# Kernel optimization log

Hardware: AMD Instinct MI355X
Metric: run time of the kernel (lower is better)

Reference implementation:

```python
import jax, jax.numpy as jnp
import numpy as np
from jax import lax

B, S, T = 32, 100, 4
NUM_C2, NUM_C3, NUM_D, DV = 500, 2000, 1000, 128


def setup_inputs():
    key = jax.random.key(0)
    ks = jax.random.split(key, 25)
    s = 0.05
    def nrm(k, shape):
        return jax.random.normal(k, shape, dtype=jnp.float32) * s
    return {
        "c2_seq": jax.random.randint(ks[0], (B, S), 0, NUM_C2),
        "c3_seq": jax.random.randint(ks[1], (B, S, T), 1, NUM_C3 + 1),  # 0 is padding; use all-valid tags
        "d_seq": jax.random.randint(ks[2], (B, S), 0, NUM_D),
        "r_seq": jax.random.randint(ks[3], (B, S), 0, 2),
        "D_emb": nrm(ks[4], (NUM_D, 1)),
        "R_emb": nrm(ks[5], (2, DV)),
        "v_c2": nrm(ks[6], (DV,)),
        "v_c3": nrm(ks[7], (DV,)),
        "v_d": nrm(ks[8], (DV,)),
        "W_ih": nrm(ks[9], (3 * DV, 2 * DV)),
        "W_hh": nrm(ks[10], (3 * DV, DV)),
        "b_ih": nrm(ks[11], (3 * DV,)),
        "b_hh": nrm(ks[12], (3 * DV,)),
        "l1_W1": nrm(ks[13], (DV, DV)), "l1_b1": nrm(ks[14], (DV,)),
        "l1_W2": nrm(ks[15], (1, DV)), "l1_b2": nrm(ks[16], (1,)),
        "l2_W1": nrm(ks[17], (DV, 4 * DV)), "l2_b1": nrm(ks[18], (DV,)),
        "l2_W2": nrm(ks[19], (1, DV)), "l2_b2": nrm(ks[20], (1,)),
        "l3_W1": nrm(ks[21], (DV, 4 * DV)), "l3_b1": nrm(ks[22], (DV,)),
        "l3_W2": nrm(ks[23], (1, DV)), "l3_b2": nrm(ks[24], (1,)),
    }


def _mlp(x, W1, b1, W2, b2):
    # Linear -> ReLU -> (Dropout: identity in eval) -> Linear -> (Dropout)
    return jnp.maximum(x @ W1.T + b1, 0.0) @ W2.T + b2


def _gru(x_seq, h0, W_ih, W_hh, b_ih, b_hh):
    # torch.nn.GRU math, batch_first
    def step(h, x):
        gi = x @ W_ih.T + b_ih
        gh = h @ W_hh.T + b_hh
        i_r, i_z, i_n = jnp.split(gi, 3, axis=-1)
        h_r, h_z, h_n = jnp.split(gh, 3, axis=-1)
        r = jax.nn.sigmoid(i_r + h_r)
        z = jax.nn.sigmoid(i_z + h_z)
        n = jnp.tanh(i_n + r * h_n)
        h_new = (1.0 - z) * n + z * h
        return h_new, h_new
    _, hs = lax.scan(step, h0, jnp.swapaxes(x_seq, 0, 1))
    return jnp.swapaxes(hs, 0, 1)


def _forward(c2_seq, c3_seq, d_seq, r_seq, p):
    (D_emb, R_emb, v_c2, v_c3, v_d, W_ih, W_hh, b_ih, b_hh,
     l1_W1, l1_b1, l1_W2, l1_b2, l2_W1, l2_b1, l2_W2, l2_b2,
     l3_W1, l3_b1, l3_W2, l3_b2) = p
    Bn = c2_seq.shape[0]
    gamma = D_emb[d_seq]                      # [B,S,1]
    v_d_seq = gamma * v_d                     # [B,S,DV]
    v_r_seq = R_emb[r_seq]                    # [B,S,DV]
    h0 = jnp.zeros((Bn, DV), dtype=v_d_seq.dtype)
    h_seq = _gru(jnp.concatenate([v_d_seq, v_r_seq], -1), h0, W_ih, W_hh, b_ih, b_hh)
    alpha_seq = _mlp(h_seq, l1_W1, l1_b1, l1_W2, l1_b2)[..., 0]   # [B,S]

    def step(carry, xs):
        C2, C3 = carry
        c2, c3, vd, vr = xs                                      # [B],[B,T],[B,DV],[B,DV]
        mask = (c3 != 0).astype(C3.dtype)                        # [B,T]
        w = mask / mask.sum(-1, keepdims=True)
        beta2 = jnp.take_along_axis(C2, c2[:, None], axis=-1)    # [B,1]
        beta3 = jnp.take_along_axis(C3, c3, axis=-1)             # [B,T]
        beta3_bar = (beta3 * w).sum(-1)                          # [B]
        vc2 = beta2 * v_c2                                       # [B,DV]
        vc3 = beta3[..., None] * v_c3                            # [B,T,DV]
        vc3_bar = beta3_bar[:, None] * v_c3                      # [B,DV]
        new_c2 = _mlp(jnp.concatenate([vc2, vc3_bar, vd, vr], -1),
                      l2_W1, l2_b1, l2_W2, l2_b2)[:, 0]          # [B]
        feat3 = jnp.concatenate([
            jnp.broadcast_to(vc2[:, None, :], vc3.shape), vc3,
            jnp.broadcast_to(vd[:, None, :], vc3.shape),
            jnp.broadcast_to(vr[:, None, :], vc3.shape)], -1)    # [B,T,4*DV]
        new_c3 = _mlp(feat3, l3_W1, l3_b1, l3_W2, l3_b2)[..., 0]  # [B,T]
        oh2 = jax.nn.one_hot(c2, NUM_C2, dtype=C2.dtype)          # [B,NC2]
        oh3 = jax.nn.one_hot(c3, NUM_C3 + 1, dtype=C3.dtype) * mask[..., None]  # [B,T,NC3+1]
        multi = oh3.sum(1)
        C2n = C2 * (1.0 - oh2) + new_c2[:, None] * oh2
        C3n = C3 * (1.0 - multi) + (new_c3[..., None] * oh3).sum(1)
        return (C2n, C3n), (C2n, C3n)

    C2_0 = jnp.zeros((Bn, NUM_C2), dtype=jnp.float32)
    C3_0 = jnp.zeros((Bn, NUM_C3 + 1), dtype=jnp.float32)
    xs = (jnp.swapaxes(c2_seq, 0, 1), jnp.swapaxes(c3_seq, 0, 1),
          jnp.swapaxes(v_d_seq, 0, 1), jnp.swapaxes(v_r_seq, 0, 1))
    _, (C2_seq, C3_seq) = lax.scan(step, (C2_0, C3_0), xs)
    C2_seq = jnp.swapaxes(C2_seq, 0, 1)   # [B,S,NUM_C2]
    C3_seq = jnp.swapaxes(C3_seq, 0, 1)   # [B,S,NUM_C3+1]
    return alpha_seq, h_seq, C2_seq, C3_seq


def reference(c2_seq, c3_seq, d_seq, r_seq, D_emb, R_emb, v_c2, v_c3, v_d,
              W_ih, W_hh, b_ih, b_hh, l1_W1, l1_b1, l1_W2, l1_b2,
              l2_W1, l2_b1, l2_W2, l2_b2, l3_W1, l3_b1, l3_W2, l3_b2):
    p = (D_emb, R_emb, v_c2, v_c3, v_d, W_ih, W_hh, b_ih, b_hh,
         l1_W1, l1_b1, l1_W2, l1_b2, l2_W1, l2_b1, l2_W2, l2_b2,
         l3_W1, l3_b1, l3_W2, l3_b2)
    return _forward(c2_seq, c3_seq, d_seq, r_seq, p)
```

## Files before the change

kernel.cpp:

```cpp
#include <hip/hip_runtime.h>

#define BB   32
#define SS   100
#define TT   4
#define NCC2 500
#define NC3P 2001
#define DD   128

#define LDSF 14664

typedef _Float16 h2v __attribute__((ext_vector_type(2)));

__device__ __forceinline__ float fast_rcp(float x) { return __builtin_amdgcn_rcpf(x); }
__device__ __forceinline__ float fast_sig(float x) { return fast_rcp(1.f + __expf(-x)); }
__device__ __forceinline__ float fast_tanh(float x) { return 1.f - 2.f * fast_rcp(__expf(2.f * x) + 1.f); }

__device__ __forceinline__ float dpp_sum64(float x) {
    x += __int_as_float(__builtin_amdgcn_update_dpp(0, __float_as_int(x), 0x111, 0xf, 0xf, true));
    x += __int_as_float(__builtin_amdgcn_update_dpp(0, __float_as_int(x), 0x112, 0xf, 0xf, true));
    x += __int_as_float(__builtin_amdgcn_update_dpp(0, __float_as_int(x), 0x114, 0xf, 0xf, true));
    x += __int_as_float(__builtin_amdgcn_update_dpp(0, __float_as_int(x), 0x118, 0xf, 0xf, true));
    x += __int_as_float(__builtin_amdgcn_update_dpp(0, __float_as_int(x), 0x142, 0xa, 0xf, true));
    x += __int_as_float(__builtin_amdgcn_update_dpp(0, __float_as_int(x), 0x143, 0xc, 0xf, true));
    return x;
}

__device__ __forceinline__ float dpp_sum16(float x) {
    x += __int_as_float(__builtin_amdgcn_update_dpp(0, __float_as_int(x), 0x111, 0xf, 0xf, true));
    x += __int_as_float(__builtin_amdgcn_update_dpp(0, __float_as_int(x), 0x112, 0xf, 0xf, true));
    x += __int_as_float(__builtin_amdgcn_update_dpp(0, __float_as_int(x), 0x114, 0xf, 0xf, true));
    x += __int_as_float(__builtin_amdgcn_update_dpp(0, __float_as_int(x), 0x118, 0xf, 0xf, true));
    return x;
}

__device__ __forceinline__ float dot4(float4 a, float4 b) {
    return fmaf(a.x, b.x, fmaf(a.y, b.y, fmaf(a.z, b.z, a.w * b.w)));
}

__device__ __forceinline__ unsigned pk16(float a, float b) {
    return __builtin_bit_cast(unsigned, __builtin_amdgcn_cvt_pkrtz(a, b));
}
__device__ __forceinline__ uint4 packf16(float4 A, float4 B) {
    uint4 u;
    u.x = pk16(A.x, A.y); u.y = pk16(A.z, A.w);
    u.z = pk16(B.x, B.y); u.w = pk16(B.z, B.w);
    return u;
}

#define MIX8(q, u, v, acc) do {                                             \
    h2v _x;                                                                 \
    _x = __builtin_bit_cast(h2v, (q).x);                                    \
    acc = fmaf((float)_x.x, (u).x, acc); acc = fmaf((float)_x.y, (u).y, acc);\
    _x = __builtin_bit_cast(h2v, (q).y);                                    \
    acc = fmaf((float)_x.x, (u).z, acc); acc = fmaf((float)_x.y, (u).w, acc);\
    _x = __builtin_bit_cast(h2v, (q).z);                                    \
    acc = fmaf((float)_x.x, (v).x, acc); acc = fmaf((float)_x.y, (v).y, acc);\
    _x = __builtin_bit_cast(h2v, (q).w);                                    \
    acc = fmaf((float)_x.x, (v).z, acc); acc = fmaf((float)_x.y, (v).w, acc);\
} while (0)

__global__ __launch_bounds__(768, 1) void k_main(
    const int* __restrict__ c2_seq, const int* __restrict__ c3_seq,
    const int* __restrict__ d_seq,  const int* __restrict__ r_seq,
    const float* __restrict__ D_emb, const float* __restrict__ Remb,
    const float* __restrict__ v_c2, const float* __restrict__ v_c3,
    const float* __restrict__ v_d,
    const float* __restrict__ W_ih, const float* __restrict__ W_hh,
    const float* __restrict__ b_ih, const float* __restrict__ b_hh,
    const float* __restrict__ l2W1, const float* __restrict__ l2b1,
    const float* __restrict__ l2W2, const float* __restrict__ l2b2,
    const float* __restrict__ l3W1, const float* __restrict__ l3b1,
    const float* __restrict__ l3W2, const float* __restrict__ l3b2,
    float* __restrict__ h_out, float* __restrict__ C2o, float* __restrict__ C3o)
{
    __shared__ __align__(16) float sh[LDSF];
    int* shi = (int*)sh;
    float4* sh4 = (float4*)sh;
    const int blk = blockIdx.x;
    const int t = threadIdx.x;

    if (blk < BB) {
        const int b  = blk;
        const int w  = t >> 6, l = t & 63;
        const int p4 = w & 3;
        const int j2 = (w >> 2) * 64 + l;
        const int jA = j2, jB = j2 + 192;
        const int kb = p4 * 32;

        uint4 wa0, wa1, wa2, wa3, wb0, wb1, wb2, wb3;
        {
            const float4* ra = (const float4*)(W_hh + jA * DD + kb);
            const float4* rb = (const float4*)(W_hh + jB * DD + kb);
            wa0 = packf16(ra[0], ra[1]); wa1 = packf16(ra[2], ra[3]);
            wa2 = packf16(ra[4], ra[5]); wa3 = packf16(ra[6], ra[7]);
            wb0 = packf16(rb[0], rb[1]); wb1 = packf16(rb[2], rb[3]);
            wb2 = packf16(rb[4], rb[5]); wb3 = packf16(rb[6], rb[7]);
        }

        {
            const float4* vd4 = (const float4*)(v_d + kb);
            const float4* r04 = (const float4*)(Remb + kb);
            const float4* r14 = (const float4*)(Remb + 128 + kb);
#pragma unroll
            for (int rr2 = 0; rr2 < 2; ++rr2) {
                const int j = rr2 ? jB : jA;
                const float4* wx = (const float4*)(W_ih + j * 256 + kb);
                const float4* wr = (const float4*)(W_ih + j * 256 + 128 + kb);
                float pd = 0.f, pr0 = 0.f, pr1 = 0.f;
#pragma unroll
                for (int i = 0; i < 8; ++i) {
                    float4 a = wx[i], c = wr[i];
                    float4 vd = vd4[i], r0 = r04[i], r1 = r14[i];
                    pd  = fmaf(a.x, vd.x, fmaf(a.y, vd.y, fmaf(a.z, vd.z, fmaf(a.w, vd.w, pd))));
                    pr0 = fmaf(c.x, r0.x, fmaf(c.y, r0.y, fmaf(c.z, r0.z, fmaf(c.w, r0.w, pr0))));
                    pr1 = fmaf(c.x, r1.x, fmaf(c.y, r1.y, fmaf(c.z, r1.z, fmaf(c.w, r1.w, pr1))));
                }
                sh[1864 + j * 4 + p4] = pd;
                sh[3400 + j * 4 + p4] = pr0;
                sh[4936 + j * 4 + p4] = pr1;
            }
        }
        if (t < SS) {
            sh[1664 + t]  = D_emb[d_seq[b * SS + t]];
            shi[1764 + t] = r_seq[b * SS + t];
        }
        __syncthreads();

        float gd_r=0,gd_z=0,gd_n=0, g0_r=0,g0_z=0,g0_n=0, g1_r=0,g1_z=0,g1_n=0;
        float bi_r=0,bi_z=0,bi_n=0, bh_r=0,bh_z=0,bh_n=0, h = 0.f;
        if (t < DD) {
            float4 a;
            a = sh4[466 + t];        gd_r = (a.x+a.y)+(a.z+a.w);
            a = sh4[466 + 128 + t];  gd_z = (a.x+a.y)+(a.z+a.w);
            a = sh4[466 + 256 + t];  gd_n = (a.x+a.y)+(a.z+a.w);
            a = sh4[850 + t];        g0_r = (a.x+a.y)+(a.z+a.w);
            a = sh4[850 + 128 + t];  g0_z = (a.x+a.y)+(a.z+a.w);
            a = sh4[850 + 256 + t];  g0_n = (a.x+a.y)+(a.z+a.w);
            a = sh4[1234 + t];       g1_r = (a.x+a.y)+(a.z+a.w);
            a = sh4[1234 + 128 + t]; g1_z = (a.x+a.y)+(a.z+a.w);
            a = sh4[1234 + 256 + t]; g1_n = (a.x+a.y)+(a.z+a.w);
            bi_r = b_ih[t]; bi_z = b_ih[t+128]; bi_n = b_ih[t+256];
            bh_r = b_hh[t]; bh_z = b_hh[t+128]; bh_n = b_hh[t+256];
            sh[t] = 0.f;
        }
        __syncthreads();

        for (int s = 0; s < SS; ++s) {
            float aA = 0.f, aB = 0.f;
            {
                const float4* hq = sh4 + p4 * 8;
                float4 h0 = hq[0], h1 = hq[1], h2 = hq[2], h3 = hq[3];
                float4 h4 = hq[4], h5 = hq[5], h6 = hq[6], h7 = hq[7];
                MIX8(wa0, h0, h1, aA); MIX8(wa1, h2, h3, aA);
                MIX8(wa2, h4, h5, aA); MIX8(wa3, h6, h7, aA);
                MIX8(wb0, h0, h1, aB); MIX8(wb1, h2, h3, aB);
                MIX8(wb2, h4, h5, aB); MIX8(wb3, h6, h7, aB);
            }
            sh[128 + jA * 4 + p4] = aA;
            sh[128 + jB * 4 + p4] = aB;
            __syncthreads();
            if (t < DD) {
                float4 q0 = sh4[32 + t];
                float4 q1 = sh4[32 + 128 + t];
                float4 q2 = sh4[32 + 256 + t];
                float ghr = (q0.x+q0.y)+(q0.z+q0.w) + bh_r;
                float ghz = (q1.x+q1.y)+(q1.z+q1.w) + bh_z;
                float ghn = (q2.x+q2.y)+(q2.z+q2.w) + bh_n;
                float gamma = sh[1664 + s]; int rr = shi[1764 + s];
                float gir = fmaf(gamma, gd_r, (rr ? g1_r : g0_r) + bi_r);
                float giz = fmaf(gamma, gd_z, (rr ? g1_z : g0_z) + bi_z);
                float gin = fmaf(gamma, gd_n, (rr ? g1_n : g0_n) + bi_n);
                float r = fast_sig(gir + ghr);
                float z = fast_sig(giz + ghz);
                float n = fast_tanh(fmaf(r, ghn, gin));
                h = (1.f - z) * n + z * h;
                sh[t] = h;
                sh[1864 + s * DD + t] = h;
            }
            __syncthreads();
        }

        {
            const float4* hs = (const float4*)(sh + 1864);
            float4* hd = (float4*)(h_out + (size_t)b * SS * DD);
            for (int i = t; i < SS * DD / 4; i += 768) hd[i] = hs[i];
        }
    } else {
        const int sb = blk - BB;
        const int b = sb >> 2;
        const int q = sb & 3;

        {
            const int g = (t & 63) >> 4, c8 = ((t & 63) & 15) * 8;
            const float* vsrc = (g == 0) ? v_c2 : (g == 1) ? v_c3 : (g == 2) ? v_d : Remb;
            const float4 va  = *(const float4*)(vsrc + c8);
            const float4 vb  = *(const float4*)(vsrc + c8 + 4);
            const float4 va1 = *(const float4*)(Remb + 128 + c8);
            const float4 vb1 = *(const float4*)(Remb + 132 + c8);
            for (int r = t >> 6; r < 256; r += 12) {
                const float* W = (r < 128) ? l2W1 : l3W1;
                float* U = sh + ((r < 128) ? 3264 : 3904);
                const int i = r & 127;
                const float* wr = W + i * 512 + g * 128 + c8;
                const float4 w0 = *(const float4*)(wr);
                const float4 w1 = *(const float4*)(wr + 4);
                float p  = dot4(w0, va)  + dot4(w1, vb);
                float p1 = dot4(w0, va1) + dot4(w1, vb1);
                p  = dpp_sum16(p);
                p1 = dpp_sum16(p1);
                if ((t & 15) == 15) {
                    U[g * 128 + i] = p;
                    if (g == 3) U[512 + i] = p1;
                }
            }
        }
        for (int k = t; k < NCC2 + NC3P; k += 768) sh[k] = 0.f;
        for (int k = t; k < SS; k += 768) {
            shi[2504 + k] = c2_seq[b * SS + k];
            sh[3004 + k]  = D_emb[d_seq[b * SS + k]];
            shi[3104 + k] = r_seq[b * SS + k];
        }
        for (int k = t; k < SS; k += 768)
            reinterpret_cast<int4*>(shi + 2604)[k] = reinterpret_cast<const int4*>(c3_seq + b * SS * TT)[k];
        __syncthreads();
        if (t >= 64) return;

        float* C2s = sh;
        float* C3s = sh + NCC2;
        const float* u2 = sh + 3264;
        const float* u3 = sh + 3904;
        const float u2a0 = u2[t],        u2a1 = u2[64 + t];
        const float u2b0 = u2[128 + t],  u2b1 = u2[192 + t];
        const float u2c0 = u2[256 + t],  u2c1 = u2[320 + t];
        const float u2d00 = u2[384 + t], u2d01 = u2[448 + t];
        const float u2d10 = u2[512 + t], u2d11 = u2[576 + t];
        const float u3a0 = u3[t],        u3a1 = u3[64 + t];
        const float u3b0 = u3[128 + t],  u3b1 = u3[192 + t];
        const float u3c0 = u3[256 + t],  u3c1 = u3[320 + t];
        const float u3d00 = u3[384 + t], u3d01 = u3[448 + t];
        const float u3d10 = u3[512 + t], u3d11 = u3[576 + t];
        const float b2_0 = l2b1[t], b2_1 = l2b1[64 + t];
        const float w2_0 = l2W2[t], w2_1 = l2W2[64 + t];
        const float b3_0 = l3b1[t], b3_1 = l3b1[64 + t];
        const float w3_0 = l3W2[t], w3_1 = l3W2[64 + t];
        const float c2bias = l2b2[0], c3bias = l3b2[0];

        int  nc2 = shi[2504];
        int4 nc3 = reinterpret_cast<const int4*>(shi + 2604)[0];
        float ngam = sh[3004];
        int   nrr  = shi[3104];

        for (int s = 0; s < SS; ++s) {
            const int rs = b * SS + s;
            const int c2i = nc2;
            const int i0 = nc3.x, i1 = nc3.y, i2 = nc3.z, i3 = nc3.w;
            const float gamma = ngam;
            const int rr = nrr;
            if (s + 1 < SS) {
                nc2 = shi[2504 + s + 1];
                nc3 = reinterpret_cast<const int4*>(shi + 2604)[s + 1];
                ngam = sh[3004 + s + 1];
                nrr  = shi[3104 + s + 1];
            }

            const float beta2 = C2s[c2i];
            const bool k0 = (i0 != 0), k1 = (i1 != 0), k2 = (i2 != 0), k3 = (i3 != 0);
            const float m0 = k0 ? 1.f : 0.f, m1 = k1 ? 1.f : 0.f;
            const float m2 = k2 ? 1.f : 0.f, m3 = k3 ? 1.f : 0.f;
            const float bt0 = C3s[i0], bt1 = C3s[i1], bt2 = C3s[i2], bt3 = C3s[i3];
            const float msum = m0 + m1 + m2 + m3;
            const float b3bar = (bt0 * m0 + bt1 * m1 + bt2 * m2 + bt3 * m3) * fast_rcp(msum);

            const float ud20 = rr ? u2d10 : u2d00, ud21 = rr ? u2d11 : u2d01;
            const float ud30 = rr ? u3d10 : u3d00, ud31 = rr ? u3d11 : u3d01;

            float h20 = fmaf(beta2, u2a0, fmaf(b3bar, u2b0, fmaf(gamma, u2c0, ud20 + b2_0)));
            float h21 = fmaf(beta2, u2a1, fmaf(b3bar, u2b1, fmaf(gamma, u2c1, ud21 + b2_1)));
            float newc2 = dpp_sum64(fmaf(fmaxf(h20, 0.f), w2_0, fmaxf(h21, 0.f) * w2_1)) + c2bias;

            const float base30 = fmaf(beta2, u3a0, fmaf(gamma, u3c0, ud30 + b3_0));
            const float base31 = fmaf(beta2, u3a1, fmaf(gamma, u3c1, ud31 + b3_1));
            float ha, hb, q0, q1, q2, q3;
            ha = fmaf(bt0, u3b0, base30); hb = fmaf(bt0, u3b1, base31);
            q0 = dpp_sum64(fmaf(fmaxf(ha, 0.f), w3_0, fmaxf(hb, 0.f) * w3_1)) + c3bias;
            ha = fmaf(bt1, u3b0, base30); hb = fmaf(bt1, u3b1, base31);
            q1 = dpp_sum64(fmaf(fmaxf(ha, 0.f), w3_0, fmaxf(hb, 0.f) * w3_1)) + c3bias;
            ha = fmaf(bt2, u3b0, base30); hb = fmaf(bt2, u3b1, base31);
            q2 = dpp_sum64(fmaf(fmaxf(ha, 0.f), w3_0, fmaxf(hb, 0.f) * w3_1)) + c3bias;
            ha = fmaf(bt3, u3b0, base30); hb = fmaf(bt3, u3b1, base31);
            q3 = dpp_sum64(fmaf(fmaxf(ha, 0.f), w3_0, fmaxf(hb, 0.f) * w3_1)) + c3bias;

            float val0, val1, val2, val3;
            {
                float c = m0 + ((k1 && i1 == i0) ? 1.f : 0.f) + ((k2 && i2 == i0) ? 1.f : 0.f) + ((k3 && i3 == i0) ? 1.f : 0.f);
                float qs = (k0 ? q0 : 0.f) + ((k1 && i1 == i0) ? q1 : 0.f) + ((k2 && i2 == i0) ? q2 : 0.f) + ((k3 && i3 == i0) ? q3 : 0.f);
                val0 = bt0 * (1.f - c) + qs;
            }
            {
                float c = ((k0 && i0 == i1) ? 1.f : 0.f) + m1 + ((k2 && i2 == i1) ? 1.f : 0.f) + ((k3 && i3 == i1) ? 1.f : 0.f);
                float qs = ((k0 && i0 == i1) ? q0 : 0.f) + (k1 ? q1 : 0.f) + ((k2 && i2 == i1) ? q2 : 0.f) + ((k3 && i3 == i1) ? q3 : 0.f);
                val1 = bt1 * (1.f - c) + qs;
            }
            {
                float c = ((k0 && i0 == i2) ? 1.f : 0.f) + ((k1 && i1 == i2) ? 1.f : 0.f) + m2 + ((k3 && i3 == i2) ? 1.f : 0.f);
                float qs = ((k0 && i0 == i2) ? q0 : 0.f) + ((k1 && i1 == i2) ? q1 : 0.f) + (k2 ? q2 : 0.f) + ((k3 && i3 == i2) ? q3 : 0.f);
                val2 = bt2 * (1.f - c) + qs;
            }
            {
                float c = ((k0 && i0 == i3) ? 1.f : 0.f) + ((k1 && i1 == i3) ? 1.f : 0.f) + ((k2 && i2 == i3) ? 1.f : 0.f) + m3;
                float qs = ((k0 && i0 == i3) ? q0 : 0.f) + ((k1 && i1 == i3) ? q1 : 0.f) + ((k2 && i2 == i3) ? q2 : 0.f) + (k3 ? q3 : 0.f);
                val3 = bt3 * (1.f - c) + qs;
            }

            if (t == 63) {
                C2s[c2i] = newc2;
                if (k0) C3s[i0] = val0;
                if (k1) C3s[i1] = val1;
                if (k2) C3s[i2] = val2;
                if (k3) C3s[i3] = val3;
            }

            if (q == 0) {
                float* c2row = C2o + (size_t)rs * NCC2;
                const float4* src = reinterpret_cast<const float4*>(C2s);
                float4* dst = reinterpret_cast<float4*>(c2row);
                dst[t] = src[t];
                if (t < 61) dst[64 + t] = src[64 + t];
            } else {
                float* c3row = C3o + (size_t)rs * NC3P;
                const int lo = (q - 1) * 667;
                const int n = 667;
                int pre = (4 - (int)(((unsigned)(rs * NC3P + lo)) & 3)) & 3;
                if (pre > n) pre = n;
                if (t < pre) c3row[lo + t] = C3s[lo + t];
                const int st = lo + pre;
                const int rem = n - pre;
                const int nv = rem >> 2, tl = rem & 3;
                for (int i = t; i < nv; i += 64) {
                    const int d = st + 4 * i;
                    *reinterpret_cast<float4*>(c3row + d) =
                        make_float4(C3s[d], C3s[d + 1], C3s[d + 2], C3s[d + 3]);
                }
                if (t < tl) {
                    const int d = st + 4 * nv + t;
                    c3row[d] = C3s[d];
                }
            }
        }
    }
}

__global__ __launch_bounds__(256) void k_alpha(const float* __restrict__ h_seq,
                                               const float* __restrict__ W1,
                                               const float* __restrict__ b1,
                                               const float* __restrict__ W2,
                                               const float* __restrict__ b2,
                                               float* __restrict__ alpha)
{
    __shared__ __align__(16) float sl[22560];
    const int t = threadIdx.x;
    const int base = blockIdx.x * 16;

    float4* hl4 = reinterpret_cast<float4*>(sl);
    const float4* hg = reinterpret_cast<const float4*>(h_seq + (size_t)base * DD);
    for (int i = t; i < 512; i += 256) hl4[i] = hg[i];

    float4* wl4 = reinterpret_cast<float4*>(sl + 6144);
    const float4* wg = reinterpret_cast<const float4*>(W1);
    for (int g = t; g < 4096; g += 256) {
        const int ch = g >> 5, k4 = g & 31;
        wl4[ch * 32 + (k4 ^ (ch & 31))] = wg[g];
    }
    __syncthreads();

    const int ch = t & 127, half = t >> 7;
    float acc[16];
#pragma unroll
    for (int r = 0; r < 16; ++r) acc[r] = 0.f;
#pragma unroll
    for (int kk = 0; kk < 16; ++kk) {
        const int k4 = half * 16 + kk;
        const float4 w = wl4[ch * 32 + (k4 ^ (ch & 31))];
#pragma unroll
        for (int r = 0; r < 16; ++r) {
            const float4 hv = hl4[r * 32 + k4];
            acc[r] = fmaf(w.x, hv.x, fmaf(w.y, hv.y, fmaf(w.z, hv.z, fmaf(w.w, hv.w, acc[r]))));
        }
    }
#pragma unroll
    for (int r = 0; r < 16; ++r) sl[2048 + r * 256 + t] = acc[r];
    __syncthreads();
    if (t < 128) {
        const float b1v = b1[t], w2v = W2[t];
#pragma unroll
        for (int r = 0; r < 16; ++r) {
            float v = fmaxf(sl[2048 + r * 256 + t] + sl[2048 + r * 256 + 128 + t] + b1v, 0.f) * w2v;
            v = dpp_sum64(v);
            if ((t & 63) == 63) sl[22528 + r * 2 + (t >> 6)] = v;
        }
    }
    __syncthreads();
    if (t < 16) alpha[base + t] = sl[22528 + 2 * t] + sl[22528 + 2 * t + 1] + b2[0];
}

extern "C" void kernel_launch(void* const* d_in, const int* in_sizes, int n_in,
                              void* d_out, int out_size, void* d_ws, size_t ws_size,
                              hipStream_t stream)
{
    (void)in_sizes; (void)n_in; (void)out_size; (void)d_ws; (void)ws_size;
    const int*   c2_seq = (const int*)d_in[0];
    const int*   c3_seq = (const int*)d_in[1];
    const int*   d_seq  = (const int*)d_in[2];
    const int*   r_seq  = (const int*)d_in[3];
    const float* D_emb  = (const float*)d_in[4];
    const float* Remb   = (const float*)d_in[5];
    const float* v_c2   = (const float*)d_in[6];
    const float* v_c3   = (const float*)d_in[7];
    const float* v_d    = (const float*)d_in[8];
    const float* W_ih   = (const float*)d_in[9];
    const float* W_hh   = (const float*)d_in[10];
    const float* b_ih   = (const float*)d_in[11];
    const float* b_hh   = (const float*)d_in[12];
    const float* l1W1   = (const float*)d_in[13];
    const float* l1b1   = (const float*)d_in[14];
    const float* l1W2   = (const float*)d_in[15];
    const float* l1b2   = (const float*)d_in[16];
    const float* l2W1   = (const float*)d_in[17];
    const float* l2b1   = (const float*)d_in[18];
    const float* l2W2   = (const float*)d_in[19];
    const float* l2b2   = (const float*)d_in[20];
    const float* l3W1   = (const float*)d_in[21];
    const float* l3b1   = (const float*)d_in[22];
    const float* l3W2   = (const float*)d_in[23];
    const float* l3b2   = (const float*)d_in[24];

    float* out   = (float*)d_out;
    float* alpha = out;
    float* h_out = out + 3200;
    float* C2o   = out + 412800;
    float* C3o   = out + 2012800;

    k_main<<<BB + 4 * BB, 768, 0, stream>>>(c2_seq, c3_seq, d_seq, r_seq, D_emb, Remb,
                                            v_c2, v_c3, v_d,
                                            W_ih, W_hh, b_ih, b_hh,
                                            l2W1, l2b1, l2W2, l2b2,
                                            l3W1, l3b1, l3W2, l3b2,
                                            h_out, C2o, C3o);
    k_alpha<<<200, 256, 0, stream>>>(h_out, l1W1, l1b1, l1W2, l1b2, alpha);
}
```

Measured before the change: 112.7 us.

## Decouple C2/C3 recurrence from row writeout and use all threads for stores

The scan blocks now run the sequential C2/C3 update on one wave and log per-step new values to LDS. Afterwards they replay those updates, and each of the four quarter-blocks writes full rows for every fourth step using all 768 threads, instead of one wave writing a column slice every step. The GRU blocks also change their partial-sum layout from interleaved float4 to a strided layout indexed by p4, and the sigmoid/tanh helpers are inlined. This is meant to take the large global writeout out of the serial dependency chain. In exchange it recomputes the same recurrence redundantly in four blocks and adds barriers inside the replay loop.

Result: slower. 118.3 us (+5.0%).

```diff
diff --git a/kernel.cpp b/kernel.cpp
--- a/kernel.cpp
+++ b/kernel.cpp
@@ -7,13 +7,11 @@
 #define NC3P 2001
 #define DD   128
 
-#define LDSF 14664
+#define LDSF 14680
 
 typedef _Float16 h2v __attribute__((ext_vector_type(2)));
 
 __device__ __forceinline__ float fast_rcp(float x) { return __builtin_amdgcn_rcpf(x); }
-__device__ __forceinline__ float fast_sig(float x) { return fast_rcp(1.f + __expf(-x)); }
-__device__ __forceinline__ float fast_tanh(float x) { return 1.f - 2.f * fast_rcp(__expf(2.f * x) + 1.f); }
 
 __device__ __forceinline__ float dpp_sum64(float x) {
     x += __int_as_float(__builtin_amdgcn_update_dpp(0, __float_as_int(x), 0x111, 0xf, 0xf, true));
@@ -115,30 +113,32 @@
                     pr0 = fmaf(c.x, r0.x, fmaf(c.y, r0.y, fmaf(c.z, r0.z, fmaf(c.w, r0.w, pr0))));
                     pr1 = fmaf(c.x, r1.x, fmaf(c.y, r1.y, fmaf(c.z, r1.z, fmaf(c.w, r1.w, pr1))));
                 }
-                sh[1864 + j * 4 + p4] = pd;
-                sh[3400 + j * 4 + p4] = pr0;
-                sh[4936 + j * 4 + p4] = pr1;
+                sh[1880 + p4 * 388 + j] = pd;
+                sh[3432 + p4 * 388 + j] = pr0;
+                sh[4984 + p4 * 388 + j] = pr1;
             }
         }
         if (t < SS) {
-            sh[1664 + t]  = D_emb[d_seq[b * SS + t]];
-            shi[1764 + t] = r_seq[b * SS + t];
+            sh[1680 + t]  = D_emb[d_seq[b * SS + t]];
+            shi[1780 + t] = r_seq[b * SS + t];
         }
         __syncthreads();
 
         float gd_r=0,gd_z=0,gd_n=0, g0_r=0,g0_z=0,g0_n=0, g1_r=0,g1_z=0,g1_n=0;
         float bi_r=0,bi_z=0,bi_n=0, bh_r=0,bh_z=0,bh_n=0, h = 0.f;
         if (t < DD) {
-            float4 a;
-            a = sh4[466 + t];        gd_r = (a.x+a.y)+(a.z+a.w);
-            a = sh4[466 + 128 + t];  gd_z = (a.x+a.y)+(a.z+a.w);
-            a = sh4[466 + 256 + t];  gd_n = (a.x+a.y)+(a.z+a.w);
-            a = sh4[850 + t];        g0_r = (a.x+a.y)+(a.z+a.w);
-            a = sh4[850 + 128 + t];  g0_z = (a.x+a.y)+(a.z+a.w);
-            a = sh4[850 + 256 + t];  g0_n = (a.x+a.y)+(a.z+a.w);
-            a = sh4[1234 + t];       g1_r = (a.x+a.y)+(a.z+a.w);
-            a = sh4[1234 + 128 + t]; g1_z = (a.x+a.y)+(a.z+a.w);
-            a = sh4[1234 + 256 + t]; g1_n = (a.x+a.y)+(a.z+a.w);
+#pragma unroll
+            for (int p = 0; p < 4; ++p) {
+                gd_r += sh[1880 + p * 388 + t];
+                gd_z += sh[1880 + p * 388 + 128 + t];
+                gd_n += sh[1880 + p * 388 + 256 + t];
+                g0_r += sh[3432 + p * 388 + t];
+                g0_z += sh[3432 + p * 388 + 128 + t];
+                g0_n += sh[3432 + p * 388 + 256 + t];
+                g1_r += sh[4984 + p * 388 + t];
+                g1_z += sh[4984 + p * 388 + 128 + t];
+                g1_n += sh[4984 + p * 388 + 256 + t];
+            }
             bi_r = b_ih[t]; bi_z = b_ih[t+128]; bi_n = b_ih[t+256];
             bh_r = b_hh[t]; bh_z = b_hh[t+128]; bh_n = b_hh[t+256];
             sh[t] = 0.f;
@@ -156,32 +156,33 @@
                 MIX8(wb0, h0, h1, aB); MIX8(wb1, h2, h3, aB);
                 MIX8(wb2, h4, h5, aB); MIX8(wb3, h6, h7, aB);
             }
-            sh[128 + jA * 4 + p4] = aA;
-            sh[128 + jB * 4 + p4] = aB;
+            sh[128 + p4 * 388 + jA] = aA;
+            sh[128 + p4 * 388 + jB] = aB;
             __syncthreads();
             if (t < DD) {
-                float4 q0 = sh4[32 + t];
-                float4 q1 = sh4[32 + 128 + t];
-                float4 q2 = sh4[32 + 256 + t];
-                float ghr = (q0.x+q0.y)+(q0.z+q0.w) + bh_r;
-                float ghz = (q1.x+q1.y)+(q1.z+q1.w) + bh_z;
-                float ghn = (q2.x+q2.y)+(q2.z+q2.w) + bh_n;
-                float gamma = sh[1664 + s]; int rr = shi[1764 + s];
+                float ghr = bh_r, ghz = bh_z, ghn = bh_n;
+#pragma unroll
+                for (int p = 0; p < 4; ++p) {
+                    ghr += sh[128 + p * 388 + t];
+                    ghz += sh[128 + p * 388 + 128 + t];
+                    ghn += sh[128 + p * 388 + 256 + t];
+                }
+                float gamma = sh[1680 + s]; int rr = shi[1780 + s];
                 float gir = fmaf(gamma, gd_r, (rr ? g1_r : g0_r) + bi_r);
                 float giz = fmaf(gamma, gd_z, (rr ? g1_z : g0_z) + bi_z);
                 float gin = fmaf(gamma, gd_n, (rr ? g1_n : g0_n) + bi_n);
-                float r = fast_sig(gir + ghr);
-                float z = fast_sig(giz + ghz);
-                float n = fast_tanh(fmaf(r, ghn, gin));
+                float r = fast_rcp(1.f + __expf(-(gir + ghr)));
+                float z = fast_rcp(1.f + __expf(-(giz + ghz)));
+                float n = 1.f - 2.f * fast_rcp(__expf(2.f * fmaf(r, ghn, gin)) + 1.f);
                 h = (1.f - z) * n + z * h;
                 sh[t] = h;
-                sh[1864 + s * DD + t] = h;
+                sh[1880 + s * DD + t] = h;
             }
             __syncthreads();
         }
 
         {
-            const float4* hs = (const float4*)(sh + 1864);
+            const float4* hs = (const float4*)(sh + 1880);
             float4* hd = (float4*)(h_out + (size_t)b * SS * DD);
             for (int i = t; i < SS * DD / 4; i += 768) hd[i] = hs[i];
         }
@@ -223,128 +224,144 @@
         for (int k = t; k < SS; k += 768)
             reinterpret_cast<int4*>(shi + 2604)[k] = reinterpret_cast<const int4*>(c3_seq + b * SS * TT)[k];
         __syncthreads();
-        if (t >= 64) return;
+
+        if (t < 64) {
+            float* C2s = sh;
+            float* C3s = sh + NCC2;
+            const float* u2 = sh + 3264;
+            const float* u3 = sh + 3904;
+            const float u2a0 = u2[t],        u2a1 = u2[64 + t];
+            const float u2b0 = u2[128 + t],  u2b1 = u2[192 + t];
+            const float u2c0 = u2[256 + t],  u2c1 = u2[320 + t];
+            const float u2d00 = u2[384 + t], u2d01 = u2[448 + t];
+            const float u2d10 = u2[512 + t], u2d11 = u2[576 + t];
+            const float u3a0 = u3[t],        u3a1 = u3[64 + t];
+            const float u3b0 = u3[128 + t],  u3b1 = u3[192 + t];
+            const float u3c0 = u3[256 + t],  u3c1 = u3[320 + t];
+            const float u3d00 = u3[384 + t], u3d01 = u3[448 + t];
+            const float u3d10 = u3[512 + t], u3d11 = u3[576 + t];
+            const float b2_0 = l2b1[t], b2_1 = l2b1[64 + t];
+            const float w2_0 = l2W2[t], w2_1 = l2W2[64 + t];
+            const float b3_0 = l3b1[t], b3_1 = l3b1[64 + t];
+            const float w3_0 = l3W2[t], w3_1 = l3W2[64 + t];
+            const float c2bias = l2b2[0], c3bias = l3b2[0];
+
+            int  nc2 = shi[2504];
+            int4 nc3 = reinterpret_cast<const int4*>(shi + 2604)[0];
+            float ngam = sh[3004];
+            int   nrr  = shi[3104];
+
+            for (int s = 0; s < SS; ++s) {
+                const int c2i = nc2;
+                const int i0 = nc3.x, i1 = nc3.y, i2 = nc3.z, i3 = nc3.w;
+                const float gamma = ngam;
+                const int rr = nrr;
+                if (s + 1 < SS) {
+                    nc2 = shi[2504 + s + 1];
+                    nc3 = reinterpret_cast<const int4*>(shi + 2604)[s + 1];
+                    ngam = sh[3004 + s + 1];
+                    nrr  = shi[3104 + s + 1];
+                }
+
+                const float beta2 = C2s[c2i];
+                const bool k0 = (i0 != 0), k1 = (i1 != 0), k2 = (i2 != 0), k3 = (i3 != 0);
+                const float m0 = k0 ? 1.f : 0.f, m1 = k1 ? 1.f : 0.f;
+                const float m2 = k2 ? 1.f : 0.f, m3 = k3 ? 1.f : 0.f;
+                const float bt0 = C3s[i0], bt1 = C3s[i1], bt2 = C3s[i2], bt3 = C3s[i3];
+                const float msum = m0 + m1 + m2 + m3;
+                const float b3bar = (bt0 * m0 + bt1 * m1 + bt2 * m2 + bt3 * m3) * fast_rcp(msum);
+
+                const float ud20 = rr ? u2d10 : u2d00, ud21 = rr ? u2d11 : u2d01;
+                const float ud30 = rr ? u3d10 : u3d00, ud31 = rr ? u3d11 : u3d01;
+
+                float h20 = fmaf(beta2, u2a0, fmaf(b3bar, u2b0, fmaf(gamma, u2c0, ud20 + b2_0)));
+                float h21 = fmaf(beta2, u2a1, fmaf(b3bar, u2b1, fmaf(gamma, u2c1, ud21 + b2_1)));
+                float newc2 = dpp_sum64(fmaf(fmaxf(h20, 0.f), w2_0, fmaxf(h21, 0.f) * w2_1)) + c2bias;
+
+                const float base30 = fmaf(beta2, u3a0, fmaf(gamma, u3c0, ud30 + b3_0));
+                const float base31 = fmaf(beta2, u3a1, fmaf(gamma, u3c1, ud31 + b3_1));
+                float ha, hb, q0, q1, q2, q3;
+                ha = fmaf(bt0, u3b0, base30); hb = fmaf(bt0, u3b1, base31);
+                q0 = dpp_sum64(fmaf(fmaxf(ha, 0.f), w3_0, fmaxf(hb, 0.f) * w3_1)) + c3bias;
+                ha = fmaf(bt1, u3b0, base30); hb = fmaf(bt1, u3b1, base31);
+                q1 = dpp_sum64(fmaf(fmaxf(ha, 0.f), w3_0, fmaxf(hb, 0.f) * w3_1)) + c3bias;
+                ha = fmaf(bt2, u3b0, base30); hb = fmaf(bt2, u3b1, base31);
+                q2 = dpp_sum64(fmaf(fmaxf(ha, 0.f), w3_0, fmaxf(hb, 0.f) * w3_1)) + c3bias;
+                ha = fmaf(bt3, u3b0, base30); hb = fmaf(bt3, u3b1, base31);
+                q3 = dpp_sum64(fmaf(fmaxf(ha, 0.f), w3_0, fmaxf(hb, 0.f) * w3_1)) + c3bias;
+
+                float val0, val1, val2, val3;
+                {
+                    float c = m0 + ((k1 && i1 == i0) ? 1.f : 0.f) + ((k2 && i2 == i0) ? 1.f : 0.f) + ((k3 && i3 == i0) ? 1.f : 0.f);
+                    float qs = (k0 ? q0 : 0.f) + ((k1 && i1 == i0) ? q1 : 0.f) + ((k2 && i2 == i0) ? q2 : 0.f) + ((k3 && i3 == i0) ? q3 : 0.f);
+                    val0 = bt0 * (1.f - c) + qs;
+                }
+                {
+                    float c = ((k0 && i0 == i1) ? 1.f : 0.f) + m1 + ((k2 && i2 == i1) ? 1.f : 0.f) + ((k3 && i3 == i1) ? 1.f : 0.f);
+                    float qs = ((k0 && i0 == i1) ? q0 : 0.f) + (k1 ? q1 : 0.f) + ((k2 && i2 == i1) ? q2 : 0.f) + ((k3 && i3 == i1) ? q3 : 0.f);
+                    val1 = bt1 * (1.f - c) + qs;
+                }
+                {
+                    float c = ((k0 && i0 == i2) ? 1.f : 0.f) + ((k1 && i1 == i2) ? 1.f : 0.f) + m2 + ((k3 && i3 == i2) ? 1.f : 0.f);
+                    float qs = ((k0 && i0 == i2) ? q0 : 0.f) + ((k1 && i1 == i2) ? q1 : 0.f) + (k2 ? q2 : 0.f) + ((k3 && i3 == i2) ? q3 : 0.f);
+                    val2 = bt2 * (1.f - c) + qs;
+                }
+                {
+                    float c = ((k0 && i0 == i3) ? 1.f : 0.f) + ((k1 && i1 == i3) ? 1.f : 0.f) + ((k2 && i2 == i3) ? 1.f : 0.f) + m3;
+                    float qs = ((k0 && i0 == i3) ? q0 : 0.f) + ((k1 && i1 == i3) ? q1 : 0.f) + ((k2 && i2 == i3) ? q2 : 0.f) + (k3 ? q3 : 0.f);
+                    val3 = bt3 * (1.f - c) + qs;
+                }
+
+                if (t == 63) {
+                    C2s[c2i] = newc2;
+                    if (k0) C3s[i0] = val0;
+                    if (k1) C3s[i1] = val1;
+                    if (k2) C3s[i2] = val2;
+                    if (k3) C3s[i3] = val3;
+                    sh[4544 + s] = newc2;
+                    sh[4644 + 4 * s + 0] = val0;
+                    sh[4644 + 4 * s + 1] = val1;
+                    sh[4644 + 4 * s + 2] = val2;
+                    sh[4644 + 4 * s + 3] = val3;
+                }
+            }
+        }
+        __syncthreads();
+
+        for (int k = t; k < NCC2 + NC3P; k += 768) sh[k] = 0.f;
+        __syncthreads();
 
         float* C2s = sh;
         float* C3s = sh + NCC2;
-        const float* u2 = sh + 3264;
-        const float* u3 = sh + 3904;
-        const float u2a0 = u2[t],        u2a1 = u2[64 + t];
-        const float u2b0 = u2[128 + t],  u2b1 = u2[192 + t];
-        const float u2c0 = u2[256 + t],  u2c1 = u2[320 + t];
-        const float u2d00 = u2[384 + t], u2d01 = u2[448 + t];
-        const float u2d10 = u2[512 + t], u2d11 = u2[576 + t];
-        const float u3a0 = u3[t],        u3a1 = u3[64 + t];
-        const float u3b0 = u3[128 + t],  u3b1 = u3[192 + t];
-        const float u3c0 = u3[256 + t],  u3c1 = u3[320 + t];
-        const float u3d00 = u3[384 + t], u3d01 = u3[448 + t];
-        const float u3d10 = u3[512 + t], u3d11 = u3[576 + t];
-        const float b2_0 = l2b1[t], b2_1 = l2b1[64 + t];
-        const float w2_0 = l2W2[t], w2_1 = l2W2[64 + t];
-        const float b3_0 = l3b1[t], b3_1 = l3b1[64 + t];
-        const float w3_0 = l3W2[t], w3_1 = l3W2[64 + t];
-        const float c2bias = l2b2[0], c3bias = l3b2[0];
-
-        int  nc2 = shi[2504];
-        int4 nc3 = reinterpret_cast<const int4*>(shi + 2604)[0];
-        float ngam = sh[3004];
-        int   nrr  = shi[3104];
-
         for (int s = 0; s < SS; ++s) {
-            const int rs = b * SS + s;
-            const int c2i = nc2;
-            const int i0 = nc3.x, i1 = nc3.y, i2 = nc3.z, i3 = nc3.w;
-            const float gamma = ngam;
-            const int rr = nrr;
-            if (s + 1 < SS) {
-                nc2 = shi[2504 + s + 1];
-                nc3 = reinterpret_cast<const int4*>(shi + 2604)[s + 1];
-                ngam = sh[3004 + s + 1];
-                nrr  = shi[3104 + s + 1];
-            }
-
-            const float beta2 = C2s[c2i];
-            const bool k0 = (i0 != 0), k1 = (i1 != 0), k2 = (i2 != 0), k3 = (i3 != 0);
-            const float m0 = k0 ? 1.f : 0.f, m1 = k1 ? 1.f : 0.f;
-            const float m2 = k2 ? 1.f : 0.f, m3 = k3 ? 1.f : 0.f;
-            const float bt0 = C3s[i0], bt1 = C3s[i1], bt2 = C3s[i2], bt3 = C3s[i3];
-            const float msum = m0 + m1 + m2 + m3;
-            const float b3bar = (bt0 * m0 + bt1 * m1 + bt2 * m2 + bt3 * m3) * fast_rcp(msum);
-
-            const float ud20 = rr ? u2d10 : u2d00, ud21 = rr ? u2d11 : u2d01;
-            const float ud30 = rr ? u3d10 : u3d00, ud31 = rr ? u3d11 : u3d01;
-
-            float h20 = fmaf(beta2, u2a0, fmaf(b3bar, u2b0, fmaf(gamma, u2c0, ud20 + b2_0)));
-            float h21 = fmaf(beta2, u2a1, fmaf(b3bar, u2b1, fmaf(gamma, u2c1, ud21 + b2_1)));
-            float newc2 = dpp_sum64(fmaf(fmaxf(h20, 0.f), w2_0, fmaxf(h21, 0.f) * w2_1)) + c2bias;
-
-            const float base30 = fmaf(beta2, u3a0, fmaf(gamma, u3c0, ud30 + b3_0));
-            const float base31 = fmaf(beta2, u3a1, fmaf(gamma, u3c1, ud31 + b3_1));
-            float ha, hb, q0, q1, q2, q3;
-            ha = fmaf(bt0, u3b0, base30); hb = fmaf(bt0, u3b1, base31);
-            q0 = dpp_sum64(fmaf(fmaxf(ha, 0.f), w3_0, fmaxf(hb, 0.f) * w3_1)) + c3bias;
-            ha = fmaf(bt1, u3b0, base30); hb = fmaf(bt1, u3b1, base31);
-            q1 = dpp_sum64(fmaf(fmaxf(ha, 0.f), w3_0, fmaxf(hb, 0.f) * w3_1)) + c3bias;
-            ha = fmaf(bt2, u3b0, base30); hb = fmaf(bt2, u3b1, base31);
-            q2 = dpp_sum64(fmaf(fmaxf(ha, 0.f), w3_0, fmaxf(hb, 0.f) * w3_1)) + c3bias;
-            ha = fmaf(bt3, u3b0, base30); hb = fmaf(bt3, u3b1, base31);
-            q3 = dpp_sum64(fmaf(fmaxf(ha, 0.f), w3_0, fmaxf(hb, 0.f) * w3_1)) + c3bias;
-
-            float val0, val1, val2, val3;
-            {
-                float c = m0 + ((k1 && i1 == i0) ? 1.f : 0.f) + ((k2 && i2 == i0) ? 1.f : 0.f) + ((k3 && i3 == i0) ? 1.f : 0.f);
-                float qs = (k0 ? q0 : 0.f) + ((k1 && i1 == i0) ? q1 : 0.f) + ((k2 && i2 == i0) ? q2 : 0.f) + ((k3 && i3 == i0) ? q3 : 0.f);
-                val0 = bt0 * (1.f - c) + qs;
-            }
-            {
-                float c = ((k0 && i0 == i1) ? 1.f : 0.f) + m1 + ((k2 && i2 == i1) ? 1.f : 0.f) + ((k3 && i3 == i1) ? 1.f : 0.f);
-                float qs = ((k0 && i0 == i1) ? q0 : 0.f) + (k1 ? q1 : 0.f) + ((k2 && i2 == i1) ? q2 : 0.f) + ((k3 && i3 == i1) ? q3 : 0.f);
-                val1 = bt1 * (1.f - c) + qs;
-            }
-            {
-                float c = ((k0 && i0 == i2) ? 1.f : 0.f) + ((k1 && i1 == i2) ? 1.f : 0.f) + m2 + ((k3 && i3 == i2) ? 1.f : 0.f);
-                float qs = ((k0 && i0 == i2) ? q0 : 0.f) + ((k1 && i1 == i2) ? q1 : 0.f) + (k2 ? q2 : 0.f) + ((k3 && i3 == i2) ? q3 : 0.f);
-                val2 = bt2 * (1.f - c) + qs;
-            }
-            {
-                float c = ((k0 && i0 == i3) ? 1.f : 0.f) + ((k1 && i1 == i3) ? 1.f : 0.f) + ((k2 && i2 == i3) ? 1.f : 0.f) + m3;
-                float qs = ((k0 && i0 == i3) ? q0 : 0.f) + ((k1 && i1 == i3) ? q1 : 0.f) + ((k2 && i2 == i3) ? q2 : 0.f) + (k3 ? q3 : 0.f);
-                val3 = bt3 * (1.f - c) + qs;
-            }
-
-            if (t == 63) {
-                C2s[c2i] = newc2;
-                if (k0) C3s[i0] = val0;
-                if (k1) C3s[i1] = val1;
-                if (k2) C3s[i2] = val2;
-                if (k3) C3s[i3] = val3;
-            }
-
-            if (q == 0) {
+            if (t == 0) {
+                C2s[shi[2504 + s]] = sh[4544 + s];
+                const int4 ic3 = reinterpret_cast<const int4*>(shi + 2604)[s];
+                if (ic3.x) C3s[ic3.x] = sh[4644 + 4 * s + 0];
+                if (ic3.y) C3s[ic3.y] = sh[4644 + 4 * s + 1];
+                if (ic3.z) C3s[ic3.z] = sh[4644 + 4 * s + 2];
+                if (ic3.w) C3s[ic3.w] = sh[4644 + 4 * s + 3];
+            }
+            if ((s & 3) == q) {
+                __syncthreads();
+                const int rs = b * SS + s;
                 float* c2row = C2o + (size_t)rs * NCC2;
-                const float4* src = reinterpret_cast<const float4*>(C2s);
-                float4* dst = reinterpret_cast<float4*>(c2row);
-                dst[t] = src[t];
-                if (t < 61) dst[64 + t] = src[64 + t];
-            } else {
+                if (t < 125) reinterpret_cast<float4*>(c2row)[t] = reinterpret_cast<const float4*>(C2s)[t];
                 float* c3row = C3o + (size_t)rs * NC3P;
-                const int lo = (q - 1) * 667;
-                const int n = 667;
-                int pre = (4 - (int)(((unsigned)(rs * NC3P + lo)) & 3)) & 3;
-                if (pre > n) pre = n;
-                if (t < pre) c3row[lo + t] = C3s[lo + t];
-                const int st = lo + pre;
-                const int rem = n - pre;
+                const int p0 = (4 - (rs & 3)) & 3;
+                if (t < p0) c3row[t] = C3s[t];
+                const int rem = NC3P - p0;
                 const int nv = rem >> 2, tl = rem & 3;
-                for (int i = t; i < nv; i += 64) {
-                    const int d = st + 4 * i;
+                if (t < nv) {
+                    const int d = p0 + 4 * t;
                     *reinterpret_cast<float4*>(c3row + d) =
                         make_float4(C3s[d], C3s[d + 1], C3s[d + 2], C3s[d + 3]);
                 }
                 if (t < tl) {
-                    const int d = st + 4 * nv + t;
+                    const int d = p0 + 4 * nv + t;
                     c3row[d] = C3s[d];
                 }
+                __syncthreads();
             }
         }
     }
```
